# Optimization experiments

Hardware: AMD Instinct MI355X
Metric: run time of the kernel (lower is better)

## Reference

```python
import jax, jax.numpy as jnp
import numpy as np

N_NODES = 8192
D = 384
N_EDGES = 262144
N_REL = 4
N_LAYERS = 2
BATCH = 64


def setup_inputs() -> dict:
    key = jax.random.key(0)
    ks = jax.random.split(key, 8)
    x = jax.random.normal(ks[0], (N_NODES, D), jnp.float32)
    edge_index = jax.random.randint(ks[1], (2, N_EDGES), 0, N_NODES, dtype=jnp.int32)
    edge_type = jax.random.randint(ks[2], (N_EDGES,), 0, N_REL, dtype=jnp.int32)
    s = 1.0 / np.sqrt(D)
    W_rel = jax.random.uniform(ks[3], (N_LAYERS, N_REL, D, D), jnp.float32, -s, s)
    b_rel = jnp.zeros((N_LAYERS, N_REL, D), jnp.float32)
    norm_const = jnp.ones((N_LAYERS, N_REL), jnp.float32)
    W_msg = jax.random.uniform(ks[4], (N_LAYERS, D, D), jnp.float32, -s, s)
    b_msg = jnp.zeros((N_LAYERS, D), jnp.float32)
    W_self = jax.random.uniform(ks[5], (N_LAYERS, D, D), jnp.float32, -s, s)
    b_self = jnp.zeros((N_LAYERS, D), jnp.float32)
    bn_gamma = jnp.ones((D,), jnp.float32)
    bn_beta = jnp.zeros((D,), jnp.float32)
    return {"x": x, "edge_index": edge_index, "edge_type": edge_type,
            "bn_gamma": bn_gamma, "bn_beta": bn_beta,
            "W_rel": W_rel, "b_rel": b_rel, "norm_const": norm_const,
            "W_msg": W_msg, "b_msg": b_msg, "W_self": W_self, "b_self": b_self,
            "batch_size": BATCH}


def _seg_sum(v, idx, n):
    return jax.ops.segment_sum(v, idx, num_segments=n)


def _forward(x, bn_gamma, bn_beta, W_rel, b_rel, norm_const, W_msg, b_msg,
             W_self, b_self, edge_index, edge_type, batch_size):
    n = x.shape[0]
    # BatchNorm1d (training-mode batch stats) on the utterance embeddings
    mu = x.mean(axis=0)
    var = x.var(axis=0)
    h = bn_gamma * (x - mu) * jax.lax.rsqrt(var + 1e-5) + bn_beta
    src, dst = edge_index[0], edge_index[1]  # PyG: row=source(j), col=target(i)
    # pairwise cosine similarity, gathered only at the edges actually used:
    # edge_weights[dst, src] = <h_dst, h_src> / (|h_dst||h_src|)
    xn = h / jnp.linalg.norm(h, axis=1, keepdims=True)
    w_e = jnp.sum(xn[dst] * xn[src], axis=-1)  # [E]
    ones_e = jnp.ones(src.shape[0], jnp.float32)
    n_layers, n_rel = W_rel.shape[0], W_rel.shape[1]
    for l in range(n_layers):
        # RelationAwareMP: per-relation linear + weighted scatter-mean, summed
        out = jnp.zeros((n, W_rel.shape[2]), h.dtype)
        for r in range(n_rel):
            mask = (edge_type == r).astype(h.dtype)  # [E]
            xr = h @ W_rel[l, r].T + b_rel[l, r]  # [N, D]
            coef = mask * w_e / norm_const[l, r]  # [E]
            s = _seg_sum(coef[:, None] * xr[src], dst, n)
            c = _seg_sum(mask, dst, n)
            out = out + s / jnp.maximum(c, 1.0)[:, None]
        rel_out = jax.nn.relu(out)
        # MP: relu(mean_j lin(x_j) + self_lin(x)), then residual
        mj = rel_out @ W_msg[l].T + b_msg[l]
        s = _seg_sum(mj[src], dst, n)
        c = _seg_sum(ones_e, dst, n)
        aggr = s / jnp.maximum(c, 1.0)[:, None]
        h = jax.nn.relu(aggr + rel_out @ W_self[l].T + b_self[l]) + h
    return h.reshape(batch_size, -1, h.shape[-1]).mean(axis=1)


def reference(x, edge_index, edge_type, bn_gamma, bn_beta, W_rel, b_rel,
              norm_const, W_msg, b_msg, W_self, b_self, batch_size):
    return _forward(x, bn_gamma, bn_beta, W_rel, b_rel, norm_const,
                    W_msg, b_msg, W_self, b_self,
                    edge_index, edge_type, batch_size)
```

## Files before the change

### kernel.cpp

```cpp
#include <hip/hip_runtime.h>
#include <hip/hip_bf16.h>

#define NN 8192
#define DD 384
#define NE 262144
#define NR 4
#define NL 2
#define NB 64

typedef __attribute__((ext_vector_type(8))) short bf16x8;
typedef __attribute__((ext_vector_type(4))) float f32x4;

__device__ __forceinline__ unsigned short f2bf(float f) {
  unsigned u = __float_as_uint(f);
  unsigned r = (u + 0x7fffu + ((u >> 16) & 1u)) >> 16;
  return (unsigned short)r;
}
__device__ __forceinline__ unsigned pack_bf2(float lo, float hi) {
  return (unsigned)f2bf(lo) | ((unsigned)f2bf(hi) << 16);
}
__device__ __forceinline__ float bflo(unsigned u) { return __uint_as_float(u << 16); }
__device__ __forceinline__ float bfhi(unsigned u) { return __uint_as_float(u & 0xffff0000u); }
__device__ __forceinline__ void gl_lds16(const void* g, void* l) {
  __builtin_amdgcn_global_load_lds(
      (const __attribute__((address_space(1))) unsigned int*)g,
      (__attribute__((address_space(3))) unsigned int*)l, 16, 0, 0);
}
__device__ __forceinline__ float dot8(uint4 a, uint4 b) {
  return bflo(a.x) * bflo(b.x) + bfhi(a.x) * bfhi(b.x) +
         bflo(a.y) * bflo(b.y) + bfhi(a.y) * bfhi(b.y) +
         bflo(a.z) * bflo(b.z) + bfhi(a.z) * bfhi(b.z) +
         bflo(a.w) * bflo(b.w) + bfhi(a.w) * bfhi(b.w);
}

__global__ void k_zero(uint4* __restrict__ p, int n4) {
  int i = blockIdx.x * 256 + threadIdx.x;
  if (i < n4) p[i] = make_uint4(0, 0, 0, 0);
}

__global__ void k_colstats(const float* __restrict__ x, float* __restrict__ musum,
                           float* __restrict__ msqsum) {
  int c = threadIdx.x;
  int r0 = blockIdx.x * 32;
  float s = 0.f, s2 = 0.f;
  for (int r = 0; r < 32; ++r) {
    float v = x[(size_t)(r0 + r) * DD + c];
    s += v; s2 += v * v;
  }
  atomicAdd(&musum[c], s);
  atomicAdd(&msqsum[c], s2);
}

__global__ void k_bn(const float* __restrict__ x, const float* __restrict__ gamma,
                     const float* __restrict__ beta, const float* __restrict__ musum,
                     const float* __restrict__ msqsum, float* __restrict__ h,
                     short* __restrict__ h_bf, float* __restrict__ ninv) {
  int n = blockIdx.x;
  int t = threadIdx.x;
  float ss = 0.f;
#pragma unroll
  for (int i = 0; i < 6; ++i) {
    int c = t + i * 64;
    float m = musum[c] * (1.f / NN);
    float var = msqsum[c] * (1.f / NN) - m * m;
    float v = gamma[c] * (x[(size_t)n * DD + c] - m) * rsqrtf(var + 1e-5f) + beta[c];
    h[(size_t)n * DD + c] = v;
    h_bf[(size_t)n * DD + c] = (short)f2bf(v);
    ss += v * v;
  }
#pragma unroll
  for (int m = 32; m; m >>= 1) ss += __shfl_xor(ss, m, 64);
  if (t == 0) ninv[n] = rsqrtf(ss);
}

__global__ void k_counts(const int* __restrict__ ei, const int* __restrict__ et,
                         int* __restrict__ c_rel) {
  int e = blockIdx.x * blockDim.x + threadIdx.x;
  if (e >= NE) return;
  int dst = ei[NE + e];
  atomicAdd(&c_rel[dst * NR + et[e]], 1);
}

__global__ void k_scan(const int* __restrict__ c_rel, int* __restrict__ rp2,
                       int* __restrict__ cursor) {
  __shared__ int part[1024];
  int t = threadIdx.x;
  int base = t * 32;
  int v[32]; int s = 0;
#pragma unroll
  for (int i = 0; i < 32; ++i) { v[i] = c_rel[base + i]; s += v[i]; }
  part[t] = s;
  __syncthreads();
  for (int off = 1; off < 1024; off <<= 1) {
    int add = (t >= off) ? part[t - off] : 0;
    __syncthreads();
    part[t] += add;
    __syncthreads();
  }
  int run = (t == 0) ? 0 : part[t - 1];
  if (t == 0) rp2[0] = 0;
#pragma unroll
  for (int i = 0; i < 32; ++i) {
    cursor[base + i] = run;
    run += v[i];
    rp2[base + i + 1] = run;
  }
}

__global__ void k_fill(const int* __restrict__ ei, const int* __restrict__ et,
                       int* __restrict__ cursor, int* __restrict__ meta) {
  int e = blockIdx.x * blockDim.x + threadIdx.x;
  if (e >= NE) return;
  int src = ei[e], dst = ei[NE + e];
  int pos = atomicAdd(&cursor[dst * NR + et[e]], 1);
  meta[pos] = src;
}

__global__ void k_we2(const short* __restrict__ hb, const float* __restrict__ ninv,
                      const int* __restrict__ rp2, const int* __restrict__ meta,
                      float* __restrict__ wsort) {
  int n = blockIdx.x;
  int g = threadIdx.x >> 4, sl = threadIdx.x & 15;
  int beg = rp2[n * 4], end = rp2[n * 4 + 4];
  if (beg == end) return;
  const uint4* hd = (const uint4*)(hb + (size_t)n * DD);
  uint4 b0 = hd[sl], b1 = hd[16 + sl], b2 = hd[32 + sl];
  float nd = ninv[n];
  for (int s = beg + g; s < end; s += 16) {
    int src = meta[s];
    const uint4* hs = (const uint4*)(hb + (size_t)src * DD);
    float acc = dot8(hs[sl], b0) + dot8(hs[16 + sl], b1) + dot8(hs[32 + sl], b2);
#pragma unroll
    for (int m = 8; m; m >>= 1) acc += __shfl_xor(acc, m, 64);
    if (sl == 0) wsort[s] = acc * ninv[src] * nd;
  }
}

__global__ void k_aggrel(const short* __restrict__ hb, const int* __restrict__ rp2,
                         const int* __restrict__ meta, const float* __restrict__ wsort,
                         const float* __restrict__ nc, short* __restrict__ Agg,
                         float* __restrict__ SC, int layer) {
  int n = blockIdx.x;
  int t = threadIdx.x;
  int r = t / 96;
  int i = t - r * 96;
  int beg = rp2[n * 4 + r], end = rp2[n * 4 + r + 1];
  float a0 = 0, a1 = 0, a2 = 0, a3 = 0, s = 0;
  int e = beg;
  for (; e + 3 < end; e += 4) {
    int s0 = meta[e], s1 = meta[e + 1], s2 = meta[e + 2], s3 = meta[e + 3];
    float w0 = wsort[e], w1 = wsort[e + 1], w2 = wsort[e + 2], w3 = wsort[e + 3];
    uint2 u0 = ((const uint2*)(hb + (size_t)s0 * DD))[i];
    uint2 u1 = ((const uint2*)(hb + (size_t)s1 * DD))[i];
    uint2 u2 = ((const uint2*)(hb + (size_t)s2 * DD))[i];
    uint2 u3 = ((const uint2*)(hb + (size_t)s3 * DD))[i];
    a0 += w0 * bflo(u0.x) + w1 * bflo(u1.x) + w2 * bflo(u2.x) + w3 * bflo(u3.x);
    a1 += w0 * bfhi(u0.x) + w1 * bfhi(u1.x) + w2 * bfhi(u2.x) + w3 * bfhi(u3.x);
    a2 += w0 * bflo(u0.y) + w1 * bflo(u1.y) + w2 * bflo(u2.y) + w3 * bflo(u3.y);
    a3 += w0 * bfhi(u0.y) + w1 * bfhi(u1.y) + w2 * bfhi(u2.y) + w3 * bfhi(u3.y);
    s += w0 + w1 + w2 + w3;
  }
  for (; e < end; ++e) {
    int s0 = meta[e];
    float w0 = wsort[e];
    uint2 u0 = ((const uint2*)(hb + (size_t)s0 * DD))[i];
    a0 += w0 * bflo(u0.x); a1 += w0 * bfhi(u0.x);
    a2 += w0 * bflo(u0.y); a3 += w0 * bfhi(u0.y);
    s += w0;
  }
  int c = end - beg;
  float f = 1.f / (nc[layer * 4 + r] * (float)(c > 1 ? c : 1));
  uint2 o;
  o.x = pack_bf2(a0 * f, a1 * f);
  o.y = pack_bf2(a2 * f, a3 * f);
  ((uint2*)(Agg + (size_t)n * 1536 + r * 384))[i] = o;
  if (i == 0) SC[n * 4 + r] = s * f;
}

__global__ void k_aggmp(short* __restrict__ B1, const int* __restrict__ rp2,
                        const int* __restrict__ meta) {
  __shared__ float red[3][96][4];
  int n = blockIdx.x;
  int t = threadIdx.x;
  int g = t / 96, i = t - g * 96;
  int beg = rp2[n * 4], end = rp2[n * 4 + 4];
  float a0 = 0, a1 = 0, a2 = 0, a3 = 0;
  int e = beg + g;
  for (; e + 12 < end; e += 16) {
    int s0 = meta[e], s1 = meta[e + 4], s2 = meta[e + 8], s3 = meta[e + 12];
    uint2 u0 = ((const uint2*)(B1 + (size_t)s0 * 768 + 384))[i];
    uint2 u1 = ((const uint2*)(B1 + (size_t)s1 * 768 + 384))[i];
    uint2 u2 = ((const uint2*)(B1 + (size_t)s2 * 768 + 384))[i];
    uint2 u3 = ((const uint2*)(B1 + (size_t)s3 * 768 + 384))[i];
    a0 += bflo(u0.x) + bflo(u1.x) + bflo(u2.x) + bflo(u3.x);
    a1 += bfhi(u0.x) + bfhi(u1.x) + bfhi(u2.x) + bfhi(u3.x);
    a2 += bflo(u0.y) + bflo(u1.y) + bflo(u2.y) + bflo(u3.y);
    a3 += bfhi(u0.y) + bfhi(u1.y) + bfhi(u2.y) + bfhi(u3.y);
  }
  for (; e < end; e += 4) {
    int s0 = meta[e];
    uint2 u = ((const uint2*)(B1 + (size_t)s0 * 768 + 384))[i];
    a0 += bflo(u.x); a1 += bfhi(u.x);
    a2 += bflo(u.y); a3 += bfhi(u.y);
  }
  if (g) {
    red[g - 1][i][0] = a0; red[g - 1][i][1] = a1;
    red[g - 1][i][2] = a2; red[g - 1][i][3] = a3;
  }
  __syncthreads();
  if (g == 0) {
#pragma unroll
    for (int k = 0; k < 3; ++k) {
      a0 += red[k][i][0]; a1 += red[k][i][1];
      a2 += red[k][i][2]; a3 += red[k][i][3];
    }
    float inv = (end > beg) ? 1.f / (float)(end - beg) : 0.f;
    uint2 o;
    o.x = pack_bf2(a0 * inv, a1 * inv);
    o.y = pack_bf2(a2 * inv, a3 * inv);
    ((uint2*)(B1 + (size_t)n * 768))[i] = o;
  }
}

__global__ void k_packall(const float* __restrict__ W_rel, const float* __restrict__ W_msg,
                          const float* __restrict__ W_self, short* __restrict__ Wcat,
                          short* __restrict__ Wcat2) {
  const int T1 = NL * 384 * 1536;
  const int T2 = NL * 384 * 768;
  int idx = blockIdx.x * blockDim.x + threadIdx.x;
  if (idx < T1) {
    int l = idx / (384 * 1536);
    int rem = idx - l * 384 * 1536;
    int i = rem / 1536, kk = rem - i * 1536;
    int r = kk / 384, k = kk - r * 384;
    Wcat[idx] = (short)f2bf(W_rel[(((size_t)(l * NR + r) * DD) + i) * DD + k]);
  } else if (idx < T1 + T2) {
    int j = idx - T1;
    int l = j / (384 * 768);
    int rem = j - l * 384 * 768;
    int i = rem / 768, kk = rem - i * 768;
    float v = (kk < 384) ? W_msg[((size_t)l * DD + i) * DD + kk]
                         : W_self[((size_t)l * DD + i) * DD + kk - 384];
    Wcat2[j] = (short)f2bf(v);
  }
}

template <int MODE>
__global__ __launch_bounds__(256) void k_gemm_mfma(
    const short* __restrict__ A, int K, const short* __restrict__ Bp,
    const float* __restrict__ SC, const float* __restrict__ brel_l,
    const float* __restrict__ bmsg_l, const float* __restrict__ bself_l,
    const int* __restrict__ rp2, float* __restrict__ h,
    short* __restrict__ h_bf, short* __restrict__ Cout) {
  __shared__ short As[2][64 * 64];
  __shared__ short Bs[2][64 * 64];
  int tid = threadIdx.x;
  int lane = tid & 63;
  int w = tid >> 6;
  int wr = w >> 1, wc = w & 1;
  int bm = blockIdx.x, bn = blockIdx.y;

  int r0 = (w << 3) + (lane >> 3);
  int qg = (lane & 7) ^ (r0 & 7);
  const short* Ag0 = A + (size_t)(bm * 64 + r0) * K + qg * 8;
  const short* Ag1 = A + (size_t)(bm * 64 + r0 + 32) * K + qg * 8;
  const short* Bg0 = Bp + (size_t)(bn * 64 + r0) * K + qg * 8;
  const short* Bg1 = Bp + (size_t)(bn * 64 + r0 + 32) * K + qg * 8;

  auto stage = [&](int bi, int k0) {
    gl_lds16(Ag0 + k0, &As[bi][w * 512]);
    gl_lds16(Ag1 + k0, &As[bi][2048 + w * 512]);
    gl_lds16(Bg0 + k0, &Bs[bi][w * 512]);
    gl_lds16(Bg1 + k0, &Bs[bi][2048 + w * 512]);
  };

  f32x4 acc[2][2] = {};
  int fr = lane & 15, fq = lane >> 4;
  int nt = K >> 6;
  stage(0, 0);
  __syncthreads();
  for (int t = 0; t < nt; ++t) {
    if (t + 1 < nt) stage((t + 1) & 1, (t + 1) << 6);
    const short* Ab = As[t & 1];
    const short* Bb = Bs[t & 1];
#pragma unroll
    for (int kk = 0; kk < 2; ++kk) {
      bf16x8 a[2], b[2];
#pragma unroll
      for (int i = 0; i < 2; ++i) {
        int r = wr * 32 + i * 16 + fr;
        int qs = (kk * 4 + fq) ^ (r & 7);
        a[i] = *(const bf16x8*)&Ab[r * 64 + qs * 8];
      }
#pragma unroll
      for (int j = 0; j < 2; ++j) {
        int r = wc * 32 + j * 16 + fr;
        int qs = (kk * 4 + fq) ^ (r & 7);
        b[j] = *(const bf16x8*)&Bb[r * 64 + qs * 8];
      }
#pragma unroll
      for (int i = 0; i < 2; ++i)
#pragma unroll
        for (int j = 0; j < 2; ++j)
          acc[i][j] = __builtin_amdgcn_mfma_f32_16x16x32_bf16(a[i], b[j], acc[i][j], 0, 0, 0);
    }
    __syncthreads();
  }

  int cr = (lane >> 4) * 4;
  int cc = lane & 15;
#pragma unroll
  for (int i = 0; i < 2; ++i) {
#pragma unroll
    for (int jj = 0; jj < 4; ++jj) {
      int row = bm * 64 + wr * 32 + i * 16 + cr + jj;
      if (MODE == 0) {
        float4 sc = *(const float4*)&SC[row * 4];
#pragma unroll
        for (int j = 0; j < 2; ++j) {
          int col = bn * 64 + wc * 32 + j * 16 + cc;
          float v = acc[i][j][jj] + sc.x * brel_l[col] + sc.y * brel_l[384 + col] +
                    sc.z * brel_l[768 + col] + sc.w * brel_l[1152 + col];
          Cout[(size_t)row * 768 + 384 + col] = (short)f2bf(fmaxf(v, 0.f));
        }
      } else {
        float bmul = (rp2[(row + 1) * 4] > rp2[row * 4]) ? 1.f : 0.f;
#pragma unroll
        for (int j = 0; j < 2; ++j) {
          int col = bn * 64 + wc * 32 + j * 16 + cc;
          float v = acc[i][j][jj] + bmul * bmsg_l[col] + bself_l[col];
          float o = fmaxf(v, 0.f) + h[(size_t)row * DD + col];
          h[(size_t)row * DD + col] = o;
          h_bf[(size_t)row * DD + col] = (short)f2bf(o);
        }
      }
    }
  }
}

__global__ void k_out(const float* __restrict__ h, float* __restrict__ out) {
  int b = blockIdx.x;
  int c = threadIdx.x;
  float s = 0.f;
  for (int j = 0; j < 128; ++j) s += h[(size_t)(b * 128 + j) * DD + c];
  out[b * DD + c] = s * (1.f / 128.f);
}

extern "C" void kernel_launch(void* const* d_in, const int* in_sizes, int n_in,
                              void* d_out, int out_size, void* d_ws, size_t ws_size,
                              hipStream_t stream) {
  const float* x      = (const float*)d_in[0];
  const int*   ei     = (const int*)d_in[1];
  const int*   et     = (const int*)d_in[2];
  const float* gamma  = (const float*)d_in[3];
  const float* beta   = (const float*)d_in[4];
  const float* W_rel  = (const float*)d_in[5];
  const float* b_rel  = (const float*)d_in[6];
  const float* nc     = (const float*)d_in[7];
  const float* W_msg  = (const float*)d_in[8];
  const float* b_msg  = (const float*)d_in[9];
  const float* W_self = (const float*)d_in[10];
  const float* b_self = (const float*)d_in[11];
  float* out = (float*)d_out;

  char* ws = (char*)d_ws;
  size_t off = 0;
  auto alloc = [&](size_t bytes) -> void* {
    void* p = ws + off;
    off = (off + bytes + 255) & ~(size_t)255;
    return p;
  };
  float* h      = (float*)alloc((size_t)NN * DD * 4);
  short* h_bf   = (short*)alloc((size_t)NN * DD * 2);
  short* Agg    = (short*)alloc((size_t)NN * 1536 * 2);
  short* B1     = (short*)alloc((size_t)NN * 768 * 2);
  short* Wcat   = (short*)alloc((size_t)NL * 384 * 1536 * 2);
  short* Wcat2  = (short*)alloc((size_t)NL * 384 * 768 * 2);
  float* SC     = (float*)alloc((size_t)NN * 4 * 4);
  int*   meta   = (int*)alloc((size_t)NE * 4);
  float* wsort  = (float*)alloc((size_t)NE * 4);
  int*   rp2    = (int*)alloc((size_t)(NN * 4 + 1) * 4);
  int*   cursor = (int*)alloc((size_t)NN * 4 * 4);
  float* ninv   = (float*)alloc((size_t)NN * 4);
  char*  zb     = (char*)alloc(134144);
  float* musum  = (float*)(zb);
  float* msqsum = (float*)(zb + 1536);
  int*   c_rel  = (int*)(zb + 3072);

  k_zero<<<(134144 / 16 + 255) / 256, 256, 0, stream>>>((uint4*)zb, 134144 / 16);
  k_colstats<<<256, 384, 0, stream>>>(x, musum, msqsum);
  k_bn<<<NN, 64, 0, stream>>>(x, gamma, beta, musum, msqsum, h, h_bf, ninv);
  k_counts<<<NE / 256, 256, 0, stream>>>(ei, et, c_rel);
  k_scan<<<1, 1024, 0, stream>>>(c_rel, rp2, cursor);
  k_fill<<<NE / 256, 256, 0, stream>>>(ei, et, cursor, meta);
  k_we2<<<NN, 256, 0, stream>>>(h_bf, ninv, rp2, meta, wsort);
  k_packall<<<(NL * 384 * 1536 + NL * 384 * 768 + 255) / 256, 256, 0, stream>>>(
      W_rel, W_msg, W_self, Wcat, Wcat2);

  for (int l = 0; l < NL; ++l) {
    k_aggrel<<<NN, 384, 0, stream>>>(h_bf, rp2, meta, wsort, nc, Agg, SC, l);
    k_gemm_mfma<0><<<dim3(128, 6), 256, 0, stream>>>(
        Agg, 1536, Wcat + (size_t)l * 384 * 1536, SC, b_rel + l * NR * DD,
        nullptr, nullptr, nullptr, nullptr, nullptr, B1);
    k_aggmp<<<NN, 384, 0, stream>>>(B1, rp2, meta);
    k_gemm_mfma<1><<<dim3(128, 6), 256, 0, stream>>>(
        B1, 768, Wcat2 + (size_t)l * 384 * 768, nullptr, nullptr,
        b_msg + l * DD, b_self + l * DD, rp2, h, h_bf, nullptr);
  }
  k_out<<<64, 384, 0, stream>>>(h, out);
}
```

Measured before the change: 304.3 us.

## Fuse edge cosine-weight computation into first-layer relation aggregation; swizzle GEMM block order

Merges the edge-weight kernel into the layer-0 relation aggregation. Each node block computes the cosine weights for its incoming edges in tiles staged through shared memory, stores them for layer 1, and consumes them immediately for the weighted gather. This removes one launch and the round-trip of the weights through global memory. The GEMMs switch to a 1D grid with a block-index swizzle, likely to spread consecutive blocks across XCDs, and the counts kernel moves earlier in the stream. The fused kernel adds block-wide syncs per tile and uses 384-thread blocks for the dot products, which may lower efficiency on high-degree nodes.

```diff
diff --git a/kernel.cpp b/kernel.cpp
--- a/kernel.cpp
+++ b/kernel.cpp
@@ -7,6 +7,7 @@
 #define NR 4
 #define NL 2
 #define NB 64
+#define MAXT 256
 
 typedef __attribute__((ext_vector_type(8))) short bf16x8;
 typedef __attribute__((ext_vector_type(4))) float f32x4;
@@ -116,24 +117,96 @@
   meta[pos] = src;
 }
 
-__global__ void k_we2(const short* __restrict__ hb, const float* __restrict__ ninv,
-                      const int* __restrict__ rp2, const int* __restrict__ meta,
-                      float* __restrict__ wsort) {
+__global__ void k_packall(const float* __restrict__ W_rel, const float* __restrict__ W_msg,
+                          const float* __restrict__ W_self, short* __restrict__ Wcat,
+                          short* __restrict__ Wcat2) {
+  const int T1 = NL * 384 * 1536;
+  const int T2 = NL * 384 * 768;
+  int idx = blockIdx.x * blockDim.x + threadIdx.x;
+  if (idx < T1) {
+    int l = idx / (384 * 1536);
+    int rem = idx - l * 384 * 1536;
+    int i = rem / 1536, kk = rem - i * 1536;
+    int r = kk / 384, k = kk - r * 384;
+    Wcat[idx] = (short)f2bf(W_rel[(((size_t)(l * NR + r) * DD) + i) * DD + k]);
+  } else if (idx < T1 + T2) {
+    int j = idx - T1;
+    int l = j / (384 * 768);
+    int rem = j - l * 384 * 768;
+    int i = rem / 768, kk = rem - i * 768;
+    float v = (kk < 384) ? W_msg[((size_t)l * DD + i) * DD + kk]
+                         : W_self[((size_t)l * DD + i) * DD + kk - 384];
+    Wcat2[j] = (short)f2bf(v);
+  }
+}
+
+__global__ void k_weagg(const short* __restrict__ hb, const float* __restrict__ ninv,
+                        const int* __restrict__ rp2, const int* __restrict__ meta,
+                        const float* __restrict__ nc, float* __restrict__ wsort,
+                        short* __restrict__ Agg, float* __restrict__ SC) {
+  __shared__ float wlds[MAXT];
+  __shared__ int mlds[MAXT];
   int n = blockIdx.x;
-  int g = threadIdx.x >> 4, sl = threadIdx.x & 15;
+  int tid = threadIdx.x;
   int beg = rp2[n * 4], end = rp2[n * 4 + 4];
-  if (beg == end) return;
+  int g = tid >> 3, sl = tid & 7;
+  int r = tid / 96, i = tid - r * 96;
+  int sb = rp2[n * 4 + r], se = rp2[n * 4 + r + 1];
+  float nd = ninv[n];
   const uint4* hd = (const uint4*)(hb + (size_t)n * DD);
-  uint4 b0 = hd[sl], b1 = hd[16 + sl], b2 = hd[32 + sl];
-  float nd = ninv[n];
-  for (int s = beg + g; s < end; s += 16) {
-    int src = meta[s];
-    const uint4* hs = (const uint4*)(hb + (size_t)src * DD);
-    float acc = dot8(hs[sl], b0) + dot8(hs[16 + sl], b1) + dot8(hs[32 + sl], b2);
-#pragma unroll
-    for (int m = 8; m; m >>= 1) acc += __shfl_xor(acc, m, 64);
-    if (sl == 0) wsort[s] = acc * ninv[src] * nd;
-  }
+  uint4 b0 = hd[sl], b1 = hd[8 + sl], b2 = hd[16 + sl];
+  uint4 b3 = hd[24 + sl], b4 = hd[32 + sl], b5 = hd[40 + sl];
+  float a0 = 0, a1 = 0, a2 = 0, a3 = 0, s = 0;
+  for (int t0 = beg; t0 < end; t0 += MAXT) {
+    int t1 = min(end, t0 + MAXT);
+    for (int e = t0 + g; e < t1; e += 48) {
+      int src = meta[e];
+      const uint4* hs = (const uint4*)(hb + (size_t)src * DD);
+      float acc = dot8(hs[sl], b0) + dot8(hs[8 + sl], b1) + dot8(hs[16 + sl], b2) +
+                  dot8(hs[24 + sl], b3) + dot8(hs[32 + sl], b4) + dot8(hs[40 + sl], b5);
+#pragma unroll
+      for (int m = 4; m; m >>= 1) acc += __shfl_xor(acc, m, 64);
+      if (sl == 0) {
+        float w = acc * ninv[src] * nd;
+        wlds[e - t0] = w;
+        mlds[e - t0] = src;
+        wsort[e] = w;
+      }
+    }
+    __syncthreads();
+    int lo = t0 > sb ? t0 : sb;
+    int hi = t1 < se ? t1 : se;
+    int e = lo;
+    for (; e + 3 < hi; e += 4) {
+      int s0 = mlds[e - t0], s1 = mlds[e + 1 - t0], s2 = mlds[e + 2 - t0], s3 = mlds[e + 3 - t0];
+      float w0 = wlds[e - t0], w1 = wlds[e + 1 - t0], w2 = wlds[e + 2 - t0], w3 = wlds[e + 3 - t0];
+      uint2 u0 = ((const uint2*)(hb + (size_t)s0 * DD))[i];
+      uint2 u1 = ((const uint2*)(hb + (size_t)s1 * DD))[i];
+      uint2 u2 = ((const uint2*)(hb + (size_t)s2 * DD))[i];
+      uint2 u3 = ((const uint2*)(hb + (size_t)s3 * DD))[i];
+      a0 += w0 * bflo(u0.x) + w1 * bflo(u1.x) + w2 * bflo(u2.x) + w3 * bflo(u3.x);
+      a1 += w0 * bfhi(u0.x) + w1 * bfhi(u1.x) + w2 * bfhi(u2.x) + w3 * bfhi(u3.x);
+      a2 += w0 * bflo(u0.y) + w1 * bflo(u1.y) + w2 * bflo(u2.y) + w3 * bflo(u3.y);
+      a3 += w0 * bfhi(u0.y) + w1 * bfhi(u1.y) + w2 * bfhi(u2.y) + w3 * bfhi(u3.y);
+      s += w0 + w1 + w2 + w3;
+    }
+    for (; e < hi; ++e) {
+      int s0 = mlds[e - t0];
+      float w0 = wlds[e - t0];
+      uint2 u0 = ((const uint2*)(hb + (size_t)s0 * DD))[i];
+      a0 += w0 * bflo(u0.x); a1 += w0 * bfhi(u0.x);
+      a2 += w0 * bflo(u0.y); a3 += w0 * bfhi(u0.y);
+      s += w0;
+    }
+    __syncthreads();
+  }
+  int c = se - sb;
+  float f = 1.f / (nc[r] * (float)(c > 1 ? c : 1));
+  uint2 o;
+  o.x = pack_bf2(a0 * f, a1 * f);
+  o.y = pack_bf2(a2 * f, a3 * f);
+  ((uint2*)(Agg + (size_t)n * 1536 + r * 384))[i] = o;
+  if (i == 0) SC[n * 4 + r] = s * f;
 }
 
 __global__ void k_aggrel(const short* __restrict__ hb, const int* __restrict__ rp2,
@@ -222,29 +295,6 @@
   }
 }
 
-__global__ void k_packall(const float* __restrict__ W_rel, const float* __restrict__ W_msg,
-                          const float* __restrict__ W_self, short* __restrict__ Wcat,
-                          short* __restrict__ Wcat2) {
-  const int T1 = NL * 384 * 1536;
-  const int T2 = NL * 384 * 768;
-  int idx = blockIdx.x * blockDim.x + threadIdx.x;
-  if (idx < T1) {
-    int l = idx / (384 * 1536);
-    int rem = idx - l * 384 * 1536;
-    int i = rem / 1536, kk = rem - i * 1536;
-    int r = kk / 384, k = kk - r * 384;
-    Wcat[idx] = (short)f2bf(W_rel[(((size_t)(l * NR + r) * DD) + i) * DD + k]);
-  } else if (idx < T1 + T2) {
-    int j = idx - T1;
-    int l = j / (384 * 768);
-    int rem = j - l * 384 * 768;
-    int i = rem / 768, kk = rem - i * 768;
-    float v = (kk < 384) ? W_msg[((size_t)l * DD + i) * DD + kk]
-                         : W_self[((size_t)l * DD + i) * DD + kk - 384];
-    Wcat2[j] = (short)f2bf(v);
-  }
-}
-
 template <int MODE>
 __global__ __launch_bounds__(256) void k_gemm_mfma(
     const short* __restrict__ A, int K, const short* __restrict__ Bp,
@@ -258,7 +308,9 @@
   int lane = tid & 63;
   int w = tid >> 6;
   int wr = w >> 1, wc = w & 1;
-  int bm = blockIdx.x, bn = blockIdx.y;
+  int bid = blockIdx.x;
+  int wg = ((bid & 7) * 96) + (bid >> 3);
+  int bm = wg / 6, bn = wg - bm * 6;
 
   int r0 = (w << 3) + (lane >> 3);
   int qg = (lane & 7) ^ (r0 & 7);
@@ -389,21 +441,24 @@
 
   k_zero<<<(134144 / 16 + 255) / 256, 256, 0, stream>>>((uint4*)zb, 134144 / 16);
   k_colstats<<<256, 384, 0, stream>>>(x, musum, msqsum);
+  k_counts<<<NE / 256, 256, 0, stream>>>(ei, et, c_rel);
   k_bn<<<NN, 64, 0, stream>>>(x, gamma, beta, musum, msqsum, h, h_bf, ninv);
-  k_counts<<<NE / 256, 256, 0, stream>>>(ei, et, c_rel);
   k_scan<<<1, 1024, 0, stream>>>(c_rel, rp2, cursor);
   k_fill<<<NE / 256, 256, 0, stream>>>(ei, et, cursor, meta);
-  k_we2<<<NN, 256, 0, stream>>>(h_bf, ninv, rp2, meta, wsort);
   k_packall<<<(NL * 384 * 1536 + NL * 384 * 768 + 255) / 256, 256, 0, stream>>>(
       W_rel, W_msg, W_self, Wcat, Wcat2);
 
   for (int l = 0; l < NL; ++l) {
-    k_aggrel<<<NN, 384, 0, stream>>>(h_bf, rp2, meta, wsort, nc, Agg, SC, l);
-    k_gemm_mfma<0><<<dim3(128, 6), 256, 0, stream>>>(
+    if (l == 0) {
+      k_weagg<<<NN, 384, 0, stream>>>(h_bf, ninv, rp2, meta, nc, wsort, Agg, SC);
+    } else {
+      k_aggrel<<<NN, 384, 0, stream>>>(h_bf, rp2, meta, wsort, nc, Agg, SC, l);
+    }
+    k_gemm_mfma<0><<<768, 256, 0, stream>>>(
         Agg, 1536, Wcat + (size_t)l * 384 * 1536, SC, b_rel + l * NR * DD,
         nullptr, nullptr, nullptr, nullptr, nullptr, B1);
     k_aggmp<<<NN, 384, 0, stream>>>(B1, rp2, meta);
-    k_gemm_mfma<1><<<dim3(128, 6), 256, 0, stream>>>(
+    k_gemm_mfma<1><<<768, 256, 0, stream>>>(
         B1, 768, Wcat2 + (size_t)l * 384 * 768, nullptr, nullptr,
         b_msg + l * DD, b_self + l * DD, rp2, h, h_bf, nullptr);
   }
```

Measured after the change: 346.7 us. 1.14x slower.
